# Optimization experiments

Measured on AMD Instinct MI355X. Metric: run time of the kernel, lower is better.

The kernel has to match this reference:

```python
import jax, jax.numpy as jnp
import numpy as np

L, B, D, H = 256, 128, 512, 512


def setup_inputs() -> dict:
    key = jax.random.key(0)
    ks = jax.random.split(key, 16)
    sx = 1.0 / np.sqrt(D)
    sh = 1.0 / np.sqrt(H)
    inp = {
        "inputs": jax.random.normal(ks[0], (L, B, D), jnp.float32),
        "Wi_x": jax.random.normal(ks[1], (H, D), jnp.float32) * sx,
        "bi_x": jax.random.normal(ks[2], (H,), jnp.float32) * sx,
        "Wi_h": jax.random.normal(ks[3], (H, H), jnp.float32) * sh,
        "bi_h": jax.random.normal(ks[4], (H,), jnp.float32) * sh,
        "Wf_x": jax.random.normal(ks[5], (H, D), jnp.float32) * sx,
        "bf_x": jax.random.normal(ks[6], (H,), jnp.float32) * sx,
        "Wf_h": jax.random.normal(ks[7], (H, H), jnp.float32) * sh,
        "bf_h": jax.random.normal(ks[8], (H,), jnp.float32) * sh,
        "Wo_x": jax.random.normal(ks[9], (H, D), jnp.float32) * sx,
        "Wo_h": jax.random.normal(ks[10], (H, H), jnp.float32) * sh,
        "Wu_x": jax.random.normal(ks[11], (H, D), jnp.float32) * sx,
        "Wu_h": jax.random.normal(ks[12], (H, H), jnp.float32) * sh,
    }
    # Random tree topology: node t's parent is a random earlier node (topological order),
    # node 0 is the root (parent = -1 -> zero parent state).
    rng = np.random.default_rng(0)
    parents = np.full((L, B), -1, dtype=np.int32)
    for t in range(1, L):
        parents[t] = rng.integers(0, t, size=B)
    inp["parents"] = jnp.asarray(parents)
    return inp


def reference(inputs, Wi_x, bi_x, Wi_h, bi_h, Wf_x, bf_x, Wf_h, bf_h,
              Wo_x, Wo_h, Wu_x, Wu_h, parents):
    Lm, Bm, _ = inputs.shape
    Hd = Wi_h.shape[0]
    batch_ar = jnp.arange(Bm)

    def step(carry, xs):
        Hbuf, Cbuf = carry  # [B, L, H] each
        x, p, t = xs        # x: [B, D], p: [B] parent node index (-1 = root), t: scalar
        valid = (p >= 0)[:, None]
        pi = jnp.maximum(p, 0)
        ph = jnp.where(valid, Hbuf[batch_ar, pi], 0.0)
        pc = jnp.where(valid, Cbuf[batch_ar, pi], 0.0)
        i = jax.nn.sigmoid(x @ Wi_x.T + bi_x + ph @ Wi_h.T + bi_h)
        f = jax.nn.sigmoid(x @ Wf_x.T + bf_x + ph @ Wf_h.T + bf_h)
        o = jax.nn.sigmoid(x @ Wo_x.T + ph @ Wo_h.T)
        u = jnp.tanh(x @ Wu_x.T + ph @ Wu_h.T)
        c = i * u + f * pc
        h = o * jnp.tanh(c)
        Hbuf = Hbuf.at[:, t].set(h)
        Cbuf = Cbuf.at[:, t].set(c)
        return (Hbuf, Cbuf), None

    init = (jnp.zeros((Bm, Lm, Hd), inputs.dtype),
            jnp.zeros((Bm, Lm, Hd), inputs.dtype))
    (Hbuf, _), _ = jax.lax.scan(step, init, (inputs, parents, jnp.arange(Lm)))
    return Hbuf  # [B, L, H], matching torch output layout
```

## Files before the change

### kernel.cpp

```cpp
#include <hip/hip_runtime.h>
#include <hip/hip_bf16.h>

static constexpr int LL = 256;
static constexpr int BB = 128;
static constexpr int HHH = 512;

typedef __attribute__((ext_vector_type(8))) short bf16x8;
typedef __attribute__((ext_vector_type(4))) float f32x4;
typedef __attribute__((ext_vector_type(8))) unsigned short u16x8;
typedef __attribute__((ext_vector_type(4))) unsigned short u16x4;

__device__ __forceinline__ unsigned short f2bf(float f) {
  union { float f; unsigned u; } v; v.f = f;
  unsigned r = (v.u + 0x7FFFu + ((v.u >> 16) & 1u)) >> 16;
  return (unsigned short)r;
}
__device__ __forceinline__ float bf2f(unsigned short s) {
  union { unsigned u; float f; } v; v.u = ((unsigned)s) << 16;
  return v.f;
}
__device__ __forceinline__ float sigm(float x) { return 1.0f / (1.0f + __expf(-x)); }
__device__ __forceinline__ float tanh_f(float x) { return 1.0f - 2.0f / (__expf(2.0f * x) + 1.0f); }

__global__ __launch_bounds__(256) void zero_flags(int* __restrict__ flag,
                                                  int* __restrict__ tick) {
  int i = blockIdx.x * 256 + threadIdx.x;
  if (i < LL * BB) flag[i] = 0;
  if (i < 16) tick[i] = 0;
}

__global__ __launch_bounds__(256) void wcast4(
    const float* __restrict__ s0, const float* __restrict__ s1,
    const float* __restrict__ s2, const float* __restrict__ s3,
    unsigned short* __restrict__ wx) {
  int gid = blockIdx.x * 256 + threadIdx.x;
  int e = gid * 4;
  int m = e >> 18;
  int off = e & 0x3FFFF;
  const float* srcs[4] = {s0, s1, s2, s3};
  float4 v = *(const float4*)(srcs[m] + off);
  u16x4 o;
  o[0] = f2bf(v.x); o[1] = f2bf(v.y); o[2] = f2bf(v.z); o[3] = f2bf(v.w);
  *(u16x4*)(wx + (size_t)m * 262144 + off) = o;
}

__global__ __launch_bounds__(256) void xcast(
    const float* __restrict__ X, unsigned short* __restrict__ Xbf) {
  size_t base = ((size_t)blockIdx.x * 256 + threadIdx.x) * 8;
  float4 v0 = *(const float4*)(X + base);
  float4 v1 = *(const float4*)(X + base + 4);
  u16x8 o;
  o[0] = f2bf(v0.x); o[1] = f2bf(v0.y); o[2] = f2bf(v0.z); o[3] = f2bf(v0.w);
  o[4] = f2bf(v1.x); o[5] = f2bf(v1.y); o[6] = f2bf(v1.z); o[7] = f2bf(v1.w);
  *(u16x8*)(Xbf + base) = o;
}

__global__ __launch_bounds__(256) void whpack(
    const float* __restrict__ Wi_h, const float* __restrict__ Wf_h,
    const float* __restrict__ Wo_h, const float* __restrict__ Wu_h,
    unsigned short* __restrict__ Whp) {
  int gid = blockIdx.x * 256 + threadIdx.x;
  int lane = gid & 63;
  int kb   = (gid >> 6) & 15;
  int n16  = (gid >> 10) & 31;
  int g    = gid >> 15;
  const float* W = (g == 0) ? Wi_h : (g == 1) ? Wf_h : (g == 2) ? Wo_h : Wu_h;
  int row = n16 * 16 + (lane & 15);
  int col = kb * 32 + (lane >> 4) * 8;
  const float4* s = (const float4*)(W + (size_t)row * 512 + col);
  float4 v0 = s[0], v1 = s[1];
  u16x8 o;
  o[0] = f2bf(v0.x); o[1] = f2bf(v0.y); o[2] = f2bf(v0.z); o[3] = f2bf(v0.w);
  o[4] = f2bf(v1.x); o[5] = f2bf(v1.y); o[6] = f2bf(v1.z); o[7] = f2bf(v1.w);
  *(u16x8*)&Whp[(size_t)gid * 8] = o;
}

__global__ __launch_bounds__(128) void levels_k(
    const int* __restrict__ parents, int* __restrict__ pairs,
    int* __restrict__ lmeta, int* __restrict__ mrows) {
  __shared__ unsigned short cnt2[128][130];
  __shared__ int off[130];
  __shared__ int maxl_sh;
  const int b = threadIdx.x;
  unsigned char mylvl[256];
  for (int l = 0; l < 130; ++l) cnt2[b][l] = 0;
  if (b == 0) maxl_sh = 0;
  __syncthreads();
  int maxl = 0;
  for (int t = 0; t < 256; ++t) {
    int p = parents[t * 128 + b];
    int l = (p < 0) ? 0 : (mylvl[p] + 1);
    if (l > 127) l = 127;
    mylvl[t] = (unsigned char)l;
    maxl = l > maxl ? l : maxl;
    cnt2[b][l]++;
  }
  atomicMax(&maxl_sh, maxl);
  __syncthreads();
  const int nlev = maxl_sh + 1;
  {
    int l = b;
    int s = 0;
    if (l < nlev) for (int bb = 0; bb < 128; ++bb) s += cnt2[bb][l];
    off[l + 1] = s;
  }
  __syncthreads();
  if (b == 0) {
    off[0] = 0;
    for (int l = 0; l < 128; ++l) off[l + 1] += off[l];
  }
  __syncthreads();
  {
    int l = b;
    if (l < nlev) {
      int run = off[l];
      for (int bb = 0; bb < 128; ++bb) {
        int c = cnt2[bb][l];
        cnt2[bb][l] = (unsigned short)run;
        run += c;
      }
    }
  }
  __syncthreads();
  for (int t = 0; t < 256; ++t) {
    int l = mylvl[t];
    int pos = cnt2[b][l]++;
    pairs[pos] = t * 128 + b;
  }
  if (b == 0) {
    int midx = 0;
    for (int l = 0; l < nlev; ++l) {
      int s = off[l], e = off[l + 1];
      for (int rb = s; rb < e; rb += 32) {
        int rc = (e - rb < 32) ? (e - rb) : 32;
        mrows[midx++] = (rb << 6) | rc;
      }
    }
    lmeta[0] = midx;
  }
}

__global__ __launch_bounds__(256) void xproj2(
    const unsigned short* __restrict__ Xbf, const unsigned short* __restrict__ Wx,
    const float* __restrict__ bi_x, const float* __restrict__ bi_h,
    const float* __restrict__ bf_x, const float* __restrict__ bf_h,
    unsigned short* __restrict__ Xpre) {
  __shared__ unsigned short As[128 * 64];
  __shared__ unsigned short Bs[128 * 64];
  const int m0 = blockIdx.x * 128;
  const int n0 = blockIdx.y * 128;
  const int tid = threadIdx.x;
  const int lane = tid & 63, w = tid >> 6;
  const int wr = w >> 1, wc = w & 1;
  const int hi = lane >> 4, l15 = lane & 15;
  f32x4 acc[4][4] = {};
  for (int kt = 0; kt < 8; ++kt) {
    const int k0 = kt * 64;
    __syncthreads();
#pragma unroll
    for (int i = 0; i < 4; ++i) {
      const int grp = i * 4 + w;
      const int unit = grp * 64 + lane;
      const int row = unit >> 3, c8p = unit & 7;
      const int c8l = c8p ^ (row & 7);
      const unsigned short* ga = Xbf + (size_t)(m0 + row) * 512 + k0 + c8l * 8;
      __builtin_amdgcn_global_load_lds(
          (const __attribute__((address_space(1))) unsigned int*)ga,
          (__attribute__((address_space(3))) unsigned int*)(As + grp * 512),
          16, 0, 0);
      const unsigned short* gb = Wx + (size_t)(n0 + row) * 512 + k0 + c8l * 8;
      __builtin_amdgcn_global_load_lds(
          (const __attribute__((address_space(1))) unsigned int*)gb,
          (__attribute__((address_space(3))) unsigned int*)(Bs + grp * 512),
          16, 0, 0);
    }
    __syncthreads();
#pragma unroll
    for (int kk = 0; kk < 2; ++kk) {
      const int kofs = kk * 32 + hi * 8;
      bf16x8 a[4], bb[4];
#pragma unroll
      for (int mi = 0; mi < 4; ++mi) {
        const int row = wr * 64 + mi * 16 + l15;
        a[mi] = *(const bf16x8*)&As[row * 64 + (kofs ^ ((row & 7) << 3))];
      }
#pragma unroll
      for (int ni = 0; ni < 4; ++ni) {
        const int row = wc * 64 + ni * 16 + l15;
        bb[ni] = *(const bf16x8*)&Bs[row * 64 + (kofs ^ ((row & 7) << 3))];
      }
#pragma unroll
      for (int mi = 0; mi < 4; ++mi)
#pragma unroll
        for (int ni = 0; ni < 4; ++ni)
          acc[mi][ni] = __builtin_amdgcn_mfma_f32_16x16x32_bf16(a[mi], bb[ni], acc[mi][ni], 0, 0, 0);
    }
  }
#pragma unroll
  for (int ni = 0; ni < 4; ++ni) {
    const int col = n0 + wc * 64 + ni * 16 + l15;
    const int g = col >> 9, hh = col & 511;
    float badd = 0.0f;
    if (g == 0) badd = bi_x[hh] + bi_h[hh];
    else if (g == 1) badd = bf_x[hh] + bf_h[hh];
#pragma unroll
    for (int mi = 0; mi < 4; ++mi) {
      const int rbase = m0 + wr * 64 + mi * 16 + hi * 4;
#pragma unroll
      for (int q = 0; q < 4; ++q)
        Xpre[(size_t)(rbase + q) * 2048 + col] = f2bf(acc[mi][ni][q] + badd);
    }
  }
}

__global__ __launch_bounds__(512, 2) void treelstm_flag(
    const unsigned short* __restrict__ Xpre,
    const unsigned short* __restrict__ Whp,
    const int* __restrict__ parents,
    const int* __restrict__ pairs,
    const int* __restrict__ lmeta,
    const int* __restrict__ mrows,
    int* __restrict__ flag,
    int* __restrict__ tick,
    float* __restrict__ Hout,
    float* __restrict__ Cbuf,
    unsigned short* __restrict__ Hbf) {
  __shared__ unsigned short phs[32][536];
  __shared__ float gbuf[4][32][66];
  __shared__ int sh_ticket;
  const int tid = threadIdx.x;
  const int lane = tid & 63, w = tid >> 6;
  const int g = w & 3, nh = w >> 2;
  const int ct = blockIdx.x & 7;
  const int mcnt = lmeta[0];
  const int hi = lane >> 4, l15 = lane & 15;

  bf16x8 wfrag[2][16];
  {
    const size_t base = (size_t)((g * 32 + ct * 4 + nh * 2) * 16) * 512 + lane * 8;
#pragma unroll
    for (int kb = 0; kb < 16; ++kb) {
      wfrag[0][kb] = *(const bf16x8*)&Whp[base + (size_t)kb * 512];
      wfrag[1][kb] = *(const bf16x8*)&Whp[base + (size_t)(16 + kb) * 512];
    }
  }
#pragma unroll
  for (int kb = 0; kb < 16; ++kb) {
    asm volatile("" : "+v"(wfrag[0][kb]));
    asm volatile("" : "+v"(wfrag[1][kb]));
  }

  while (true) {
    __syncthreads();
    if (tid == 0) sh_ticket = atomicAdd(&tick[ct], 1);
    __syncthreads();
    const int my = sh_ticket;
    if (my >= mcnt) break;
    const int mr = mrows[my];
    const int rbase = mr >> 6;
    const int rcnt = mr & 63;

    const int r = tid >> 4;
    const int q16 = tid & 15;
    const int hc = q16 * 4;
    const int h = ct * 64 + hc;
    int node = 0, p = -1, b = 0;
    if (r < rcnt) {
      node = pairs[rbase + r];
      p = parents[node];
      b = node & 127;
    }
    u16x4 xga[4] = {};
    if (r < rcnt) {
#pragma unroll
      for (int gg = 0; gg < 4; ++gg)
        xga[gg] = *(const u16x4*)(Xpre + (size_t)node * 2048 + gg * 512 + h);
    }

    if (tid < 32) {
      int pn = -1;
      if (tid < rcnt) {
        const int node2 = pairs[rbase + tid];
        const int p2 = parents[node2];
        if (p2 >= 0) pn = p2 * 128 + (node2 & 127);
      }
      if (pn >= 0) {
        while (__hip_atomic_load(&flag[pn], __ATOMIC_RELAXED,
                                 __HIP_MEMORY_SCOPE_AGENT) < 8)
          __builtin_amdgcn_s_sleep(1);
      }
    }
    __syncthreads();

    float4 pc = make_float4(0.f, 0.f, 0.f, 0.f);
    if (r < rcnt && p >= 0)
      pc = *(const float4*)(Cbuf + ((size_t)b * LL + p) * HHH + h);
    if (p >= 0) {
      const unsigned short* src = Hbf + ((size_t)b * LL + p) * HHH + q16 * 32;
#pragma unroll
      for (int j = 0; j < 4; ++j)
        *(u16x8*)&phs[r][q16 * 32 + j * 8] = ((const u16x8*)src)[j];
    } else {
      u16x8 z = {};
#pragma unroll
      for (int j = 0; j < 4; ++j) *(u16x8*)&phs[r][q16 * 32 + j * 8] = z;
    }
    __syncthreads();

    f32x4 acc[2][2] = {};
#pragma unroll
    for (int kb = 0; kb < 16; ++kb) {
      const int ko = kb * 32 + 8 * hi;
      bf16x8 a0 = *(const bf16x8*)&phs[l15][ko];
      bf16x8 a1 = *(const bf16x8*)&phs[16 + l15][ko];
      acc[0][0] = __builtin_amdgcn_mfma_f32_16x16x32_bf16(a0, wfrag[0][kb], acc[0][0], 0, 0, 0);
      acc[1][0] = __builtin_amdgcn_mfma_f32_16x16x32_bf16(a1, wfrag[0][kb], acc[1][0], 0, 0, 0);
      acc[0][1] = __builtin_amdgcn_mfma_f32_16x16x32_bf16(a0, wfrag[1][kb], acc[0][1], 0, 0, 0);
      acc[1][1] = __builtin_amdgcn_mfma_f32_16x16x32_bf16(a1, wfrag[1][kb], acc[1][1], 0, 0, 0);
    }
#pragma unroll
    for (int mi = 0; mi < 2; ++mi)
#pragma unroll
      for (int ni = 0; ni < 2; ++ni)
#pragma unroll
        for (int qq = 0; qq < 4; ++qq)
          gbuf[g][mi * 16 + hi * 4 + qq][nh * 32 + ni * 16 + l15] = acc[mi][ni][qq];
    __syncthreads();

    if (r < rcnt) {
      const int t = node >> 7;
      float xg[4][4];
#pragma unroll
      for (int gg = 0; gg < 4; ++gg)
#pragma unroll
        for (int j = 0; j < 4; ++j) xg[gg][j] = bf2f(xga[gg][j]);
      const float pcv[4] = {pc.x, pc.y, pc.z, pc.w};
      float cva[4], hva[4];
#pragma unroll
      for (int j = 0; j < 4; ++j) {
        float iv = sigm(gbuf[0][r][hc + j] + xg[0][j]);
        float fv = sigm(gbuf[1][r][hc + j] + xg[1][j]);
        float ov = sigm(gbuf[2][r][hc + j] + xg[2][j]);
        float uv = tanh_f(gbuf[3][r][hc + j] + xg[3][j]);
        float cv = iv * uv + fv * pcv[j];
        cva[j] = cv;
        hva[j] = ov * tanh_f(cv);
      }
      const size_t obase = ((size_t)b * LL + t) * HHH + h;
      *(float4*)(Hout + obase) = make_float4(hva[0], hva[1], hva[2], hva[3]);
      union { float f[4]; unsigned long long u[2]; } cvu;
      cvu.f[0] = cva[0]; cvu.f[1] = cva[1]; cvu.f[2] = cva[2]; cvu.f[3] = cva[3];
      unsigned long long* cp = (unsigned long long*)(Cbuf + obase);
      __hip_atomic_store(cp, cvu.u[0], __ATOMIC_RELAXED, __HIP_MEMORY_SCOPE_AGENT);
      __hip_atomic_store(cp + 1, cvu.u[1], __ATOMIC_RELAXED, __HIP_MEMORY_SCOPE_AGENT);
      union { unsigned short s[4]; unsigned long long u; } hbu;
      hbu.s[0] = f2bf(hva[0]); hbu.s[1] = f2bf(hva[1]);
      hbu.s[2] = f2bf(hva[2]); hbu.s[3] = f2bf(hva[3]);
      __hip_atomic_store((unsigned long long*)(Hbf + obase), hbu.u,
                         __ATOMIC_RELAXED, __HIP_MEMORY_SCOPE_AGENT);
    }
    asm volatile("s_waitcnt vmcnt(0)" ::: "memory");
    if (r < rcnt && q16 == 0)
      __hip_atomic_fetch_add(&flag[node], 1, __ATOMIC_RELAXED,
                             __HIP_MEMORY_SCOPE_AGENT);
  }
}

extern "C" void kernel_launch(void* const* d_in, const int* in_sizes, int n_in,
                              void* d_out, int out_size, void* d_ws, size_t ws_size,
                              hipStream_t stream) {
  const float* X    = (const float*)d_in[0];
  const float* Wi_x = (const float*)d_in[1];
  const float* bi_x = (const float*)d_in[2];
  const float* Wi_h = (const float*)d_in[3];
  const float* bi_h = (const float*)d_in[4];
  const float* Wf_x = (const float*)d_in[5];
  const float* bf_x = (const float*)d_in[6];
  const float* Wf_h = (const float*)d_in[7];
  const float* bf_h = (const float*)d_in[8];
  const float* Wo_x = (const float*)d_in[9];
  const float* Wo_h = (const float*)d_in[10];
  const float* Wu_x = (const float*)d_in[11];
  const float* Wu_h = (const float*)d_in[12];
  const int* parents = (const int*)d_in[13];
  float* Hout = (float*)d_out;

  char* ws = (char*)d_ws;
  unsigned short* Xpre = (unsigned short*)ws; ws += (size_t)32768 * 2048 * 2;
  unsigned short* Hbf  = (unsigned short*)ws; ws += (size_t)BB * LL * HHH * 2;
  float*          Cbuf = (float*)ws;          ws += (size_t)BB * LL * HHH * 4;
  unsigned short* Wxbf = (unsigned short*)ws; ws += (size_t)2048 * 512 * 2;
  unsigned short* Whp  = (unsigned short*)ws; ws += (size_t)2048 * 512 * 2;
  int*            pairs = (int*)ws;           ws += (size_t)32768 * 4;
  int*            lmeta = (int*)ws;           ws += 256 * 4;
  int*            mrows = (int*)ws;           ws += 4096 * 4;
  int*            flag  = (int*)ws;           ws += (size_t)32768 * 4;
  int*            tick  = (int*)ws;           ws += 64 * 4;
  unsigned short* Xbf = (unsigned short*)Cbuf;

  zero_flags<<<128, 256, 0, stream>>>(flag, tick);
  wcast4<<<1024, 256, 0, stream>>>(Wi_x, Wf_x, Wo_x, Wu_x, Wxbf);
  xcast<<<8192, 256, 0, stream>>>(X, Xbf);
  whpack<<<512, 256, 0, stream>>>(Wi_h, Wf_h, Wo_h, Wu_h, Whp);
  levels_k<<<1, 128, 0, stream>>>(parents, pairs, lmeta, mrows);
  dim3 g1(256, 16);
  xproj2<<<g1, 256, 0, stream>>>(Xbf, Wxbf, bi_x, bi_h, bf_x, bf_h, Xpre);

  treelstm_flag<<<512, 512, 0, stream>>>(Xpre, Whp, parents, pairs, lmeta,
                                         mrows, flag, tick, Hout, Cbuf, Hbf);
}
```

Baseline: 590.0 us.

## Merge prep kernels, fuse X cast into projection, static tree-LSTM scheduling

Folds the zero-flag, weight-cast, weight-pack and level-sort kernels into one prep launch. The separate X bf16 cast pass is removed: the projection GEMM now loads fp32 X, converts it in registers and writes the swizzled bf16 tile to LDS itself. The recurrent kernel drops the atomic ticket dispenser for a static round-robin assignment of row blocks, launches 256 blocks instead of 512, and moves the Hout store after the flag signal. These changes cut launch count, an intermediate X buffer round-trip and atomic contention, but the static schedule may load-balance worse and the synchronous X load loses the async global-to-LDS copy.

```diff
diff --git a/kernel.cpp b/kernel.cpp
--- a/kernel.cpp
+++ b/kernel.cpp
@@ -22,126 +22,117 @@
 __device__ __forceinline__ float sigm(float x) { return 1.0f / (1.0f + __expf(-x)); }
 __device__ __forceinline__ float tanh_f(float x) { return 1.0f - 2.0f / (__expf(2.0f * x) + 1.0f); }
 
-__global__ __launch_bounds__(256) void zero_flags(int* __restrict__ flag,
-                                                  int* __restrict__ tick) {
-  int i = blockIdx.x * 256 + threadIdx.x;
-  if (i < LL * BB) flag[i] = 0;
-  if (i < 16) tick[i] = 0;
-}
-
-__global__ __launch_bounds__(256) void wcast4(
+__global__ __launch_bounds__(256) void prep(
     const float* __restrict__ s0, const float* __restrict__ s1,
     const float* __restrict__ s2, const float* __restrict__ s3,
-    unsigned short* __restrict__ wx) {
-  int gid = blockIdx.x * 256 + threadIdx.x;
-  int e = gid * 4;
-  int m = e >> 18;
-  int off = e & 0x3FFFF;
-  const float* srcs[4] = {s0, s1, s2, s3};
-  float4 v = *(const float4*)(srcs[m] + off);
-  u16x4 o;
-  o[0] = f2bf(v.x); o[1] = f2bf(v.y); o[2] = f2bf(v.z); o[3] = f2bf(v.w);
-  *(u16x4*)(wx + (size_t)m * 262144 + off) = o;
-}
-
-__global__ __launch_bounds__(256) void xcast(
-    const float* __restrict__ X, unsigned short* __restrict__ Xbf) {
-  size_t base = ((size_t)blockIdx.x * 256 + threadIdx.x) * 8;
-  float4 v0 = *(const float4*)(X + base);
-  float4 v1 = *(const float4*)(X + base + 4);
-  u16x8 o;
-  o[0] = f2bf(v0.x); o[1] = f2bf(v0.y); o[2] = f2bf(v0.z); o[3] = f2bf(v0.w);
-  o[4] = f2bf(v1.x); o[5] = f2bf(v1.y); o[6] = f2bf(v1.z); o[7] = f2bf(v1.w);
-  *(u16x8*)(Xbf + base) = o;
-}
-
-__global__ __launch_bounds__(256) void whpack(
-    const float* __restrict__ Wi_h, const float* __restrict__ Wf_h,
-    const float* __restrict__ Wo_h, const float* __restrict__ Wu_h,
-    unsigned short* __restrict__ Whp) {
-  int gid = blockIdx.x * 256 + threadIdx.x;
-  int lane = gid & 63;
-  int kb   = (gid >> 6) & 15;
-  int n16  = (gid >> 10) & 31;
-  int g    = gid >> 15;
-  const float* W = (g == 0) ? Wi_h : (g == 1) ? Wf_h : (g == 2) ? Wo_h : Wu_h;
-  int row = n16 * 16 + (lane & 15);
-  int col = kb * 32 + (lane >> 4) * 8;
-  const float4* s = (const float4*)(W + (size_t)row * 512 + col);
-  float4 v0 = s[0], v1 = s[1];
-  u16x8 o;
-  o[0] = f2bf(v0.x); o[1] = f2bf(v0.y); o[2] = f2bf(v0.z); o[3] = f2bf(v0.w);
-  o[4] = f2bf(v1.x); o[5] = f2bf(v1.y); o[6] = f2bf(v1.z); o[7] = f2bf(v1.w);
-  *(u16x8*)&Whp[(size_t)gid * 8] = o;
-}
-
-__global__ __launch_bounds__(128) void levels_k(
-    const int* __restrict__ parents, int* __restrict__ pairs,
-    int* __restrict__ lmeta, int* __restrict__ mrows) {
-  __shared__ unsigned short cnt2[128][130];
-  __shared__ int off[130];
-  __shared__ int maxl_sh;
-  const int b = threadIdx.x;
-  unsigned char mylvl[256];
-  for (int l = 0; l < 130; ++l) cnt2[b][l] = 0;
-  if (b == 0) maxl_sh = 0;
-  __syncthreads();
-  int maxl = 0;
-  for (int t = 0; t < 256; ++t) {
-    int p = parents[t * 128 + b];
-    int l = (p < 0) ? 0 : (mylvl[p] + 1);
-    if (l > 127) l = 127;
-    mylvl[t] = (unsigned char)l;
-    maxl = l > maxl ? l : maxl;
-    cnt2[b][l]++;
-  }
-  atomicMax(&maxl_sh, maxl);
-  __syncthreads();
-  const int nlev = maxl_sh + 1;
-  {
-    int l = b;
-    int s = 0;
-    if (l < nlev) for (int bb = 0; bb < 128; ++bb) s += cnt2[bb][l];
-    off[l + 1] = s;
-  }
-  __syncthreads();
-  if (b == 0) {
-    off[0] = 0;
-    for (int l = 0; l < 128; ++l) off[l + 1] += off[l];
-  }
-  __syncthreads();
-  {
-    int l = b;
-    if (l < nlev) {
-      int run = off[l];
-      for (int bb = 0; bb < 128; ++bb) {
-        int c = cnt2[bb][l];
-        cnt2[bb][l] = (unsigned short)run;
-        run += c;
-      }
-    }
-  }
-  __syncthreads();
-  for (int t = 0; t < 256; ++t) {
-    int l = mylvl[t];
-    int pos = cnt2[b][l]++;
-    pairs[pos] = t * 128 + b;
-  }
-  if (b == 0) {
-    int midx = 0;
-    for (int l = 0; l < nlev; ++l) {
-      int s = off[l], e = off[l + 1];
-      for (int rb = s; rb < e; rb += 32) {
-        int rc = (e - rb < 32) ? (e - rb) : 32;
-        mrows[midx++] = (rb << 6) | rc;
-      }
-    }
-    lmeta[0] = midx;
-  }
-}
-
-__global__ __launch_bounds__(256) void xproj2(
-    const unsigned short* __restrict__ Xbf, const unsigned short* __restrict__ Wx,
+    const float* __restrict__ h0, const float* __restrict__ h1,
+    const float* __restrict__ h2, const float* __restrict__ h3,
+    const int* __restrict__ parents,
+    unsigned short* __restrict__ wx, unsigned short* __restrict__ whp,
+    int* __restrict__ pairs, int* __restrict__ lmeta, int* __restrict__ mrows,
+    int* __restrict__ flag) {
+  const int blk = blockIdx.x;
+  const int tid = threadIdx.x;
+  if (blk < 1024) {
+    int gid = blk * 256 + tid;
+    int e = gid * 4;
+    int m = e >> 18;
+    int off = e & 0x3FFFF;
+    const float* srcs[4] = {s0, s1, s2, s3};
+    float4 v = *(const float4*)(srcs[m] + off);
+    u16x4 o;
+    o[0] = f2bf(v.x); o[1] = f2bf(v.y); o[2] = f2bf(v.z); o[3] = f2bf(v.w);
+    *(u16x4*)(wx + (size_t)m * 262144 + off) = o;
+  } else if (blk < 1536) {
+    int gid = (blk - 1024) * 256 + tid;
+    int lane = gid & 63;
+    int kb   = (gid >> 6) & 15;
+    int n16  = (gid >> 10) & 31;
+    int g    = gid >> 15;
+    const float* W = (g == 0) ? h0 : (g == 1) ? h1 : (g == 2) ? h2 : h3;
+    int row = n16 * 16 + (lane & 15);
+    int col = kb * 32 + (lane >> 4) * 8;
+    const float4* s = (const float4*)(W + (size_t)row * 512 + col);
+    float4 v0 = s[0], v1 = s[1];
+    u16x8 o;
+    o[0] = f2bf(v0.x); o[1] = f2bf(v0.y); o[2] = f2bf(v0.z); o[3] = f2bf(v0.w);
+    o[4] = f2bf(v1.x); o[5] = f2bf(v1.y); o[6] = f2bf(v1.z); o[7] = f2bf(v1.w);
+    *(u16x8*)&whp[(size_t)gid * 8] = o;
+  } else if (blk == 1536) {
+    __shared__ unsigned short cnt2[128][130];
+    __shared__ int off[130];
+    __shared__ int maxl_sh;
+    const int b = tid;
+    unsigned char mylvl[256];
+    if (b < 128) {
+      for (int l = 0; l < 130; ++l) cnt2[b][l] = 0;
+    }
+    if (b == 0) maxl_sh = 0;
+    __syncthreads();
+    if (b < 128) {
+      int maxl = 0;
+      for (int t = 0; t < 256; ++t) {
+        int p = parents[t * 128 + b];
+        int l = (p < 0) ? 0 : (mylvl[p] + 1);
+        if (l > 127) l = 127;
+        mylvl[t] = (unsigned char)l;
+        maxl = l > maxl ? l : maxl;
+        cnt2[b][l]++;
+      }
+      atomicMax(&maxl_sh, maxl);
+    }
+    __syncthreads();
+    const int nlev = maxl_sh + 1;
+    if (b < 128) {
+      int l = b;
+      int s = 0;
+      if (l < nlev) for (int bb = 0; bb < 128; ++bb) s += cnt2[bb][l];
+      off[l + 1] = s;
+    }
+    __syncthreads();
+    if (b == 0) {
+      off[0] = 0;
+      for (int l = 0; l < 128; ++l) off[l + 1] += off[l];
+    }
+    __syncthreads();
+    if (b < 128) {
+      int l = b;
+      if (l < nlev) {
+        int run = off[l];
+        for (int bb = 0; bb < 128; ++bb) {
+          int c = cnt2[bb][l];
+          cnt2[bb][l] = (unsigned short)run;
+          run += c;
+        }
+      }
+    }
+    __syncthreads();
+    if (b < 128) {
+      for (int t = 0; t < 256; ++t) {
+        int l = mylvl[t];
+        int pos = cnt2[b][l]++;
+        pairs[pos] = t * 128 + b;
+      }
+    }
+    if (b == 0) {
+      int midx = 0;
+      for (int l = 0; l < nlev; ++l) {
+        int s = off[l], e = off[l + 1];
+        for (int rb = s; rb < e; rb += 32) {
+          int rc = (e - rb < 32) ? (e - rb) : 32;
+          mrows[midx++] = (rb << 6) | rc;
+        }
+      }
+      lmeta[0] = midx;
+    }
+  } else {
+    int i = (blk - 1537) * 256 + tid;
+    if (i < LL * BB) flag[i] = 0;
+  }
+}
+
+__global__ __launch_bounds__(256) void xproj3(
+    const float* __restrict__ X, const unsigned short* __restrict__ Wx,
     const float* __restrict__ bi_x, const float* __restrict__ bi_h,
     const float* __restrict__ bf_x, const float* __restrict__ bf_h,
     unsigned short* __restrict__ Xpre) {
@@ -163,16 +154,23 @@
       const int unit = grp * 64 + lane;
       const int row = unit >> 3, c8p = unit & 7;
       const int c8l = c8p ^ (row & 7);
-      const unsigned short* ga = Xbf + (size_t)(m0 + row) * 512 + k0 + c8l * 8;
-      __builtin_amdgcn_global_load_lds(
-          (const __attribute__((address_space(1))) unsigned int*)ga,
-          (__attribute__((address_space(3))) unsigned int*)(As + grp * 512),
-          16, 0, 0);
       const unsigned short* gb = Wx + (size_t)(n0 + row) * 512 + k0 + c8l * 8;
       __builtin_amdgcn_global_load_lds(
           (const __attribute__((address_space(1))) unsigned int*)gb,
           (__attribute__((address_space(3))) unsigned int*)(Bs + grp * 512),
           16, 0, 0);
+    }
+#pragma unroll
+    for (int i = 0; i < 4; ++i) {
+      const int unit = i * 256 + tid;
+      const int row = unit >> 3, c8l = unit & 7;
+      const float* src = X + (size_t)(m0 + row) * 512 + k0 + c8l * 8;
+      float4 v0 = ((const float4*)src)[0];
+      float4 v1 = ((const float4*)src)[1];
+      u16x8 o;
+      o[0] = f2bf(v0.x); o[1] = f2bf(v0.y); o[2] = f2bf(v0.z); o[3] = f2bf(v0.w);
+      o[4] = f2bf(v1.x); o[5] = f2bf(v1.y); o[6] = f2bf(v1.z); o[7] = f2bf(v1.w);
+      *(u16x8*)&As[row * 64 + ((c8l ^ (row & 7)) << 3)] = o;
     }
     __syncthreads();
 #pragma unroll
@@ -213,7 +211,7 @@
   }
 }
 
-__global__ __launch_bounds__(512, 2) void treelstm_flag(
+__global__ __launch_bounds__(512, 2) void treelstm_static(
     const unsigned short* __restrict__ Xpre,
     const unsigned short* __restrict__ Whp,
     const int* __restrict__ parents,
@@ -221,17 +219,16 @@
     const int* __restrict__ lmeta,
     const int* __restrict__ mrows,
     int* __restrict__ flag,
-    int* __restrict__ tick,
     float* __restrict__ Hout,
     float* __restrict__ Cbuf,
     unsigned short* __restrict__ Hbf) {
   __shared__ unsigned short phs[32][536];
   __shared__ float gbuf[4][32][66];
-  __shared__ int sh_ticket;
   const int tid = threadIdx.x;
   const int lane = tid & 63, w = tid >> 6;
   const int g = w & 3, nh = w >> 2;
   const int ct = blockIdx.x & 7;
+  const int slot = blockIdx.x >> 3;
   const int mcnt = lmeta[0];
   const int hi = lane >> 4, l15 = lane & 15;
 
@@ -250,12 +247,7 @@
     asm volatile("" : "+v"(wfrag[1][kb]));
   }
 
-  while (true) {
-    __syncthreads();
-    if (tid == 0) sh_ticket = atomicAdd(&tick[ct], 1);
-    __syncthreads();
-    const int my = sh_ticket;
-    if (my >= mcnt) break;
+  for (int my = slot; my < mcnt; my += 32) {
     const int mr = mrows[my];
     const int rbase = mr >> 6;
     const int rcnt = mr & 63;
@@ -327,6 +319,8 @@
           gbuf[g][mi * 16 + hi * 4 + qq][nh * 32 + ni * 16 + l15] = acc[mi][ni][qq];
     __syncthreads();
 
+    float hva[4];
+    size_t obase = 0;
     if (r < rcnt) {
       const int t = node >> 7;
       float xg[4][4];
@@ -335,7 +329,7 @@
 #pragma unroll
         for (int j = 0; j < 4; ++j) xg[gg][j] = bf2f(xga[gg][j]);
       const float pcv[4] = {pc.x, pc.y, pc.z, pc.w};
-      float cva[4], hva[4];
+      float cva[4];
 #pragma unroll
       for (int j = 0; j < 4; ++j) {
         float iv = sigm(gbuf[0][r][hc + j] + xg[0][j]);
@@ -346,8 +340,7 @@
         cva[j] = cv;
         hva[j] = ov * tanh_f(cv);
       }
-      const size_t obase = ((size_t)b * LL + t) * HHH + h;
-      *(float4*)(Hout + obase) = make_float4(hva[0], hva[1], hva[2], hva[3]);
+      obase = ((size_t)b * LL + t) * HHH + h;
       union { float f[4]; unsigned long long u[2]; } cvu;
       cvu.f[0] = cva[0]; cvu.f[1] = cva[1]; cvu.f[2] = cva[2]; cvu.f[3] = cva[3];
       unsigned long long* cp = (unsigned long long*)(Cbuf + obase);
@@ -363,6 +356,9 @@
     if (r < rcnt && q16 == 0)
       __hip_atomic_fetch_add(&flag[node], 1, __ATOMIC_RELAXED,
                              __HIP_MEMORY_SCOPE_AGENT);
+    if (r < rcnt)
+      *(float4*)(Hout + obase) = make_float4(hva[0], hva[1], hva[2], hva[3]);
+    __syncthreads();
   }
 }
 
@@ -395,17 +391,13 @@
   int*            lmeta = (int*)ws;           ws += 256 * 4;
   int*            mrows = (int*)ws;           ws += 4096 * 4;
   int*            flag  = (int*)ws;           ws += (size_t)32768 * 4;
-  int*            tick  = (int*)ws;           ws += 64 * 4;
-  unsigned short* Xbf = (unsigned short*)Cbuf;
-
-  zero_flags<<<128, 256, 0, stream>>>(flag, tick);
-  wcast4<<<1024, 256, 0, stream>>>(Wi_x, Wf_x, Wo_x, Wu_x, Wxbf);
-  xcast<<<8192, 256, 0, stream>>>(X, Xbf);
-  whpack<<<512, 256, 0, stream>>>(Wi_h, Wf_h, Wo_h, Wu_h, Whp);
-  levels_k<<<1, 128, 0, stream>>>(parents, pairs, lmeta, mrows);
+
+  prep<<<1665, 256, 0, stream>>>(Wi_x, Wf_x, Wo_x, Wu_x,
+                                 Wi_h, Wf_h, Wo_h, Wu_h,
+                                 parents, Wxbf, Whp, pairs, lmeta, mrows, flag);
   dim3 g1(256, 16);
-  xproj2<<<g1, 256, 0, stream>>>(Xbf, Wxbf, bi_x, bi_h, bf_x, bf_h, Xpre);
-
-  treelstm_flag<<<512, 512, 0, stream>>>(Xpre, Whp, parents, pairs, lmeta,
-                                         mrows, flag, tick, Hout, Cbuf, Hbf);
-}
+  xproj3<<<g1, 256, 0, stream>>>(X, Wxbf, bi_x, bi_h, bf_x, bf_h, Xpre);
+
+  treelstm_static<<<256, 512, 0, stream>>>(Xpre, Whp, parents, pairs, lmeta,
+                                           mrows, flag, Hout, Cbuf, Hbf);
+}
```

Measured after the change: 610.8 us. +3.5%, slower.
